# Kernel optimization log

Hardware: AMD Instinct MI355X
Metric: run time of the kernel (lower is better)

The kernel has to match this reference:

```python
import jax, jax.numpy as jnp
import numpy as np

NC, NPR, E, B = 200000, 100000, 500000, 200000
DIN, HID, HEADS = 16, 256, 8
D = HID // HEADS
NCOLOR, NSIZE, NGROUP = 1000, 30, 50


def setup_inputs() -> dict:
    key = jax.random.key(0)
    ks = jax.random.split(key, 24)
    g = lambda i, shape, s=0.05: jax.random.normal(ks[i], shape, jnp.float32) * s
    return dict(
        customer_x=g(0, (NC, DIN), 1.0),
        product_x=g(1, (NPR, DIN), 1.0),
        proj_cust_W=g(2, (DIN, HID)), proj_cust_b=jnp.zeros((HID,), jnp.float32),
        proj_prod_W=g(3, (DIN, HID)), proj_prod_b=jnp.zeros((HID,), jnp.float32),
        att_src_r=g(4, (HEADS, D)), att_dst_r=g(5, (HEADS, D)),
        att_src_rb=g(6, (HEADS, D)), att_dst_rb=g(7, (HEADS, D)),
        q_sem=g(8, (HID,)), k_lin_W=g(9, (HID, HID)), k_lin_b=jnp.zeros((HID,), jnp.float32),
        color_emb=g(10, (NCOLOR, 8), 1.0),
        size_emb=g(11, (NSIZE, 4), 1.0),
        group_emb=g(12, (NGROUP, 4), 1.0),
        fc1_W=g(13, (HID * 2 + 16, 128)), fc1_b=jnp.zeros((128,), jnp.float32),
        fc2_W=g(14, (128, 32)), fc2_b=jnp.zeros((32,), jnp.float32),
        fc3_W=g(15, (32, 1)), fc3_b=jnp.zeros((1,), jnp.float32),
        bn1_gamma=jnp.ones((128,), jnp.float32), bn1_beta=jnp.zeros((128,), jnp.float32),
        bn2_gamma=jnp.ones((32,), jnp.float32), bn2_beta=jnp.zeros((32,), jnp.float32),
        edge_src=jax.random.randint(ks[16], (E,), 0, NC),
        edge_dst=jax.random.randint(ks[17], (E,), 0, NPR),
        label_src=jax.random.randint(ks[18], (B,), 0, NC),
        label_dst=jax.random.randint(ks[19], (B,), 0, NPR),
        size_idx=jax.random.randint(ks[20], (B,), 0, NSIZE),
        color_idx=jax.random.randint(ks[21], (B,), 0, NCOLOR),
        group_idx=jax.random.randint(ks[22], (B,), 0, NGROUP),
    )


def _edge_softmax(logits, dst, n):
    # destination-grouped softmax over edges; logits: [E,H]
    m = jax.ops.segment_max(logits, dst, num_segments=n)
    m = jnp.where(jnp.isfinite(m), m, 0.0)
    e = jnp.exp(logits - m[dst])
    s = jax.ops.segment_sum(e, dst, num_segments=n)
    return e / (s[dst] + 1e-16)


def _han_relation(h_src, h_dst, a_src, a_dst, src, dst, n_dst):
    # h_*: [N,H,D]; a_*: [H,D]
    logits = (h_src * a_src).sum(-1)[src] + (h_dst * a_dst).sum(-1)[dst]  # [E,H]
    logits = jax.nn.leaky_relu(logits, 0.2)
    alpha = _edge_softmax(logits, dst, n_dst)
    msg = alpha[:, :, None] * h_src[src]  # [E,H,D]
    out = jax.ops.segment_sum(msg, dst, num_segments=n_dst)
    return jax.nn.relu(out.reshape(n_dst, -1))  # [N_dst, H*D]


def _group(outs, q, kW, kb):
    # semantic attention over metapaths (PyG HANConv group)
    stk = jnp.stack(outs)  # [M,N,F]
    score = (q * jnp.tanh(stk @ kW + kb).mean(1)).sum(-1)  # [M]
    attn = jax.nn.softmax(score)
    return jnp.einsum('m,mnf->nf', attn, stk)


def _bn(x, gamma, beta):
    mu = x.mean(0)
    var = x.var(0)
    return (x - mu) * jax.lax.rsqrt(var + 1e-5) * gamma + beta


def reference(customer_x, product_x, proj_cust_W, proj_cust_b, proj_prod_W, proj_prod_b,
              att_src_r, att_dst_r, att_src_rb, att_dst_rb, q_sem, k_lin_W, k_lin_b,
              color_emb, size_emb, group_emb, fc1_W, fc1_b, fc2_W, fc2_b, fc3_W, fc3_b,
              bn1_gamma, bn1_beta, bn2_gamma, bn2_beta,
              edge_src, edge_dst, label_src, label_dst, size_idx, color_idx, group_idx):
    h_c = (customer_x @ proj_cust_W + proj_cust_b).reshape(-1, HEADS, D)
    h_p = (product_x @ proj_prod_W + proj_prod_b).reshape(-1, HEADS, D)
    # relation customer -returns-> product
    out_p = _han_relation(h_c, h_p, att_src_r, att_dst_r, edge_src, edge_dst, NPR)
    # relation product -returned_by-> customer (reversed edges)
    out_c = _han_relation(h_p, h_c, att_src_rb, att_dst_rb, edge_dst, edge_src, NC)
    cust = _group([out_c], q_sem, k_lin_W, k_lin_b)  # [NC, 256]
    prod = _group([out_p], q_sem, k_lin_W, k_lin_b)  # [NPR, 256]
    feat = jnp.concatenate([cust[label_src], prod[label_dst],
                            size_emb[size_idx], color_emb[color_idx], group_emb[group_idx]], axis=-1)
    x = jax.nn.relu(feat @ fc1_W + fc1_b)
    x = _bn(x, bn1_gamma, bn1_beta)
    x = jax.nn.relu(x @ fc2_W + fc2_b)
    x = _bn(x, bn2_gamma, bn2_beta)
    return x @ fc3_W + fc3_b
```

## Files before the change

### kernel.cpp

```cpp
#include <hip/hip_runtime.h>

#define NCC 200000
#define NPRR 100000
#define NEE 500000
#define NBB 200000

typedef __attribute__((ext_vector_type(8))) short bf16x8;
typedef __attribute__((ext_vector_type(16))) float f32x16;

__device__ __forceinline__ float b2f(unsigned short u){ return __uint_as_float(((unsigned)u)<<16); }
__device__ __forceinline__ unsigned short f2b(float f){
  unsigned x = __float_as_uint(f);
  return (unsigned short)((x + 0x7fffu + ((x>>16)&1u)) >> 16);
}

__global__ __launch_bounds__(256) void wa_prep2(
    const float* __restrict__ Wc, const float* __restrict__ bc,
    const float* __restrict__ attAc, const float* __restrict__ attBc,
    const float* __restrict__ Wp, const float* __restrict__ bp,
    const float* __restrict__ attAp, const float* __restrict__ attBp,
    float* __restrict__ WAc, float* __restrict__ WAp)
{
  int tid = threadIdx.x;
  for (int task = tid; task < 4*17*8; task += 256) {
    int grp = task / 136, rem = task % 136;
    int k = rem >> 3, h = rem & 7;
    const float* att = (grp==0)?attAc:(grp==1)?attBc:(grp==2)?attAp:attBp;
    const float* W   = (grp<2)?Wc:Wp;
    const float* bias= (grp<2)?bc:bp;
    const float* row = (k < 16) ? (W + k*256) : bias;
    float acc = 0.f;
    for (int d = 0; d < 32; d++) acc = fmaf(row[h*32+d], att[h*32+d], acc);
    if (grp<2) WAc[(grp&1)*136 + rem] = acc;
    else       WAp[(grp&1)*136 + rem] = acc;
  }
}

__global__ __launch_bounds__(256) void prep_proj(
// ... 17 lines not shown
    const float* __restrict__ group_emb,
    unsigned short* __restrict__ BtC, unsigned short* __restrict__ BtP,
    float* __restrict__ Ts, float* __restrict__ Tc, float* __restrict__ Tg)
{
  int idx = blockIdx.x*256 + threadIdx.x;
  if (idx < 32768){
    int n = idx>>8, k = idx&255;
    BtC[idx] = f2b(fc1W[k*128 + n]);
  } else if (idx < 65536){
    int t = idx - 32768;
    int n = t>>8, k = t&255;
    BtP[t] = f2b(fc1W[(256+k)*128 + n]);
  } else if (idx < 65536 + 30*128){
    int t = idx - 65536;
    int s = t>>7, j = t&127;
    float a = fc1b[j];
    #pragma unroll
    for (int c=0;c<4;c++) a = fmaf(size_emb[s*4+c], fc1W[(512+c)*128+j], a);
    Ts[t] = a;
  } else if (idx < 65536 + 30*128 + 1000*128){
    int t = idx - 65536 - 30*128;
    int col = t>>7, j = t&127;
    float a = 0.f;
    #pragma unroll
    for (int c=0;c<8;c++) a = fmaf(color_emb[col*8+c], fc1W[(516+c)*128+j], a);
    Tc[t] = a;
  } else if (idx < 65536 + 30*128 + 1000*128 + 50*128){
    int t = idx - 65536 - 30*128 - 1000*128;
    int g = t>>7, j = t&127;
    float a = 0.f;
    #pragma unroll
    for (int c=0;c<4;c++) a = fmaf(group_emb[g*4+c], fc1W[(524+c)*128+j], a);
    Tg[t] = a;
  }
}

__global__ __launch_bounds__(256) void proj_mfma(const float* __restrict__ X,
    const unsigned short* __restrict__ Wt, const unsigned short* __restrict__ WAt,
    const float* __restrict__ WA,
    unsigned short* __restrict__ H, float* __restrict__ sA, float* __restrict__ sB,
    int N, int nt)
{
  __shared__ unsigned short wt[4608];
  __shared__ float biasS[16];
  int tid = threadIdx.x;
  for (int i=tid; i<512; i+=256) ((uint4*)wt)[i] = ((const uint4*)Wt)[i];
  for (int i=tid; i<64;  i+=256) ((uint4*)(wt+4096))[i] = ((const uint4*)WAt)[i];
  if (tid < 16) biasS[tid] = WA[(tid>>3)*136 + 128 + (tid&7)];
  __syncthreads();
  int wv = tid>>6, lane = tid&63, m = lane&31, hi = lane>>5;
  for (int t = blockIdx.x; t < nt; t += gridDim.x){
    int node = t*32 + m;
    bf16x8 a;
    {
      const float4* xr = (const float4*)(X + (long long)node*16 + hi*8);
      float4 f0 = xr[0], f1 = xr[1];
      unsigned short av[8] = {f2b(f0.x),f2b(f0.y),f2b(f0.z),f2b(f0.w),
                              f2b(f1.x),f2b(f1.y),f2b(f1.z),f2b(f1.w)};
      a = *(bf16x8*)av;
    }
    #pragma unroll
    for (int s=0;s<2;s++){
      int c0 = wv*64 + s*32;
      bf16x8 b = *(const bf16x8*)(wt + (c0+m)*16 + hi*8);
      f32x16 acc;
      #pragma unroll
      for (int i=0;i<16;i++) acc[i]=0.f;
      acc = __builtin_amdgcn_mfma_f32_32x32x16_bf16(a, b, acc, 0, 0, 0);
      #pragma unroll
      for (int reg=0; reg<16; reg++){
        int row = (reg&3) + 8*(reg>>2) + 4*hi;
        H[(long long)(t*32+row)*256 + c0 + m] = f2b(acc[reg]);
      }
    }
    if (wv == 0){
      bf16x8 b = *(const bf16x8*)(wt + 4096 + m*16 + hi*8);
      f32x16 acc;
      #pragma unroll
      for (int i=0;i<16;i++) acc[i]=0.f;
      acc = __builtin_amdgcn_mfma_f32_32x32x16_bf16(a, b, acc, 0, 0, 0);
      if (m < 16){
        float bias = biasS[m];
        float* dst = (m < 8) ? sA : sB;
        int h = m & 7;
        #pragma unroll
        for (int reg=0; reg<16; reg++){
          int row = (reg&3) + 8*(reg>>2) + 4*hi;
          dst[(long long)(t*32+row)*8 + h] = acc[reg] + bias;
        }
      }
    }
  }
}

__global__ __launch_bounds__(256) void hist2u(const int* __restrict__ src, const int* __restrict__ dst,
    int* __restrict__ cnt_c, int* __restrict__ cnt_p, int E,
    const int* __restrict__ lsrc, const int* __restrict__ ldst,
    int* __restrict__ used_c, int* __restrict__ used_p, int B)
{
  int e = blockIdx.x*256 + threadIdx.x;
  if (e < E){
    atomicAdd(&cnt_p[dst[e]], 1);
    atomicAdd(&cnt_c[src[e]], 1);
  }
  if (e < B){
    used_c[lsrc[e]] = 1;
    used_p[ldst[e]] = 1;
  }
}

__global__ __launch_bounds__(256) void scan_p1f(const int* __restrict__ cnt_p, int* __restrict__ bsum_p, int Np,
    const int* __restrict__ cnt_c, int* __restrict__ bsum_c, int Nc, int BP)
{
  __shared__ int red[256];
  const int* cnt; int* bsum; int N; int blk;
  if ((int)blockIdx.x < BP){ cnt=cnt_p; bsum=bsum_p; N=Np; blk=blockIdx.x; }
  else                     { cnt=cnt_c; bsum=bsum_c; N=Nc; blk=blockIdx.x-BP; }
  int tid = threadIdx.x;
  int base = blk*1024 + tid*4;
  int s = 0;
  #pragma unroll
  for (int k=0;k<4;k++){ int i=base+k; if (i<N) s += cnt[i]; }
  red[tid] = s;
  __syncthreads();
  for (int off=128; off>0; off>>=1){ if (tid<off) red[tid]+=red[tid+off]; __syncthreads(); }
  if (tid==0) bsum[blk] = red[0];
}

__global__ __launch_bounds__(256) void scan_p2f(int* __restrict__ bsum_p, int Bp, int* __restrict__ rowptr_p, int Np,
    int* __restrict__ bsum_c, int Bc, int* __restrict__ rowptr_c, int Nc)
{
  __shared__ int ts[256];
  int* bsum; int B; int* rowptr; int N;
  if (blockIdx.x == 0){ bsum=bsum_p; B=Bp; rowptr=rowptr_p; N=Np; }
  else                { bsum=bsum_c; B=Bc; rowptr=rowptr_c; N=Nc; }
  int tid = threadIdx.x;
  int v = (tid<B) ? bsum[tid] : 0;
  ts[tid] = v;
  __syncthreads();
  for (int off=1; off<256; off<<=1){
    int t = (tid>=off) ? ts[tid-off] : 0;
    __syncthreads();
    ts[tid] += t;
    __syncthreads();
  }
  if (tid < B) bsum[tid] = ts[tid] - v;
  if (tid == B-1) rowptr[N] = ts[tid];
}

__global__ __launch_bounds__(256) void scan_p3f(const int* __restrict__ cnt_p, const int* __restrict__ bsum_p,
    int* __restrict__ rowptr_p, int Np,
    const int* __restrict__ cnt_c, const int* __restrict__ bsum_c,
    int* __restrict__ rowptr_c, int Nc, int BP)
{
  __shared__ int ts[256];
  const int* cnt; const int* bsum; int* rowptr; int N; int blk;
  if ((int)blockIdx.x < BP){ cnt=cnt_p; bsum=bsum_p; rowptr=rowptr_p; N=Np; blk=blockIdx.x; }
  else                     { cnt=cnt_c; bsum=bsum_c; rowptr=rowptr_c; N=Nc; blk=blockIdx.x-BP; }
  int tid = threadIdx.x;
  int base = blk*1024 + tid*4;
  int v[4]; int s = 0;
  #pragma unroll
  for (int k=0;k<4;k++){ int i=base+k; v[k] = (i<N) ? cnt[i] : 0; s += v[k]; }
  ts[tid] = s;
  __syncthreads();
  for (int off=1; off<256; off<<=1){
    int t = (tid>=off) ? ts[tid-off] : 0;
    __syncthreads();
    ts[tid] += t;
    __syncthreads();
  }
  int run = bsum[blk] + ts[tid] - s;
  #pragma unroll
  for (int k=0;k<4;k++){ int i=base+k; if (i<N){ rowptr[i]=run; run += v[k]; } }
}

__global__ __launch_bounds__(256) void place2(const int* __restrict__ src, const int* __restrict__ dst,
    const int* __restrict__ rp_r, const int* __restrict__ rp_rb,
    int* __restrict__ cnt_p, int* __restrict__ cnt_c,
    int* __restrict__ si_r, int* __restrict__ si_rb, int E)
{
  int e = blockIdx.x*256 + threadIdx.x;
  if (e >= E) return;
  int s = src[e], d = dst[e];
  si_r [rp_r [d] + atomicAdd(&cnt_p[d], 1)] = s;
  si_rb[rp_rb[s] + atomicAdd(&cnt_c[s], 1)] = d;
}

__global__ __launch_bounds__(256) void compact2(
    const int* __restrict__ used_p, const int* __restrict__ rowptr_p, int Np,
    int4* __restrict__ list_p, int* __restrict__ lcnt_p,
    const int* __restrict__ used_c, const int* __restrict__ rowptr_c, int Nc,
    int4* __restrict__ list_c, int* __restrict__ lcnt_c)
{
  int n = blockIdx.x*256 + threadIdx.x;
  if (n < Np && used_p[n]){
    int slot = atomicAdd(lcnt_p, 1);
    list_p[slot] = make_int4(n, rowptr_p[n], rowptr_p[n+1], 0);
  }
  if (n < Nc && used_c[n]){
    int slot = atomicAdd(lcnt_c, 1);
    list_c[slot] = make_int4(n, rowptr_c[n], rowptr_c[n+1], 0);
  }
}

__global__ __launch_bounds__(256) void agg_gemm(
    const int4* __restrict__ list, const int* __restrict__ lcnt,
    const int* __restrict__ srcidx,
    const float* __restrict__ sSrc, const float* __restrict__ sDst,
    const unsigned short* __restrict__ H, const unsigned short* __restrict__ Bt,
    unsigned short* __restrict__ Y)
{
  __shared__ unsigned short feat[32*264];
  __shared__ int nid[32];
  int cnt = *lcnt;
  int base = blockIdx.x*32;
  if (base >= cnt) return;
  int tid = threadIdx.x;
  int wv = tid>>6, lane = tid&63;
  int g = lane>>4, ln = lane&15, h = ln>>1;
  #pragma unroll
  for (int t=0;t<2;t++){
    int r = wv*8 + t*4 + g;
    int slot = base + r;
    float acc[16];
    #pragma unroll
    for (int c=0;c<16;c++) acc[c]=0.f;
    float den = 0.f;
    int node = -1, e0 = 0, e1 = 0;
    if (slot < cnt){
      int4 L = list[slot];
      node = L.x; e0 = L.y; e1 = L.z;
    }
    if (ln == 0) nid[r] = node;
    if (node >= 0 && e1 > e0){
      int elast = e1 - 1;
      float sdh = sDst[(long long)node*8 + h];
      for (int e = e0; e < e1; e += 4){
        int i1 = min(e+1, elast), i2 = min(e+2, elast), i3 = min(e+3, elast);
        int s0 = srcidx[e],  s1 = srcidx[i1];
        int s2 = srcidx[i2], s3 = srcidx[i3];
        const uint4* p0 = (const uint4*)&H[(long long)s0*256 + ln*16];
        const uint4* p1 = (const uint4*)&H[(long long)s1*256 + ln*16];
        const uint4* p2 = (const uint4*)&H[(long long)s2*256 + ln*16];
        const uint4* p3 = (const uint4*)&H[(long long)s3*256 + ln*16];
        uint4 uA0 = p0[0], uA1 = p0[1];
        uint4 uB0 = p1[0], uB1 = p1[1];
        uint4 uC0 = p2[0], uC1 = p2[1];
        uint4 uD0 = p3[0], uD1 = p3[1];
        float l0 = sSrc[(long long)s0*8 + h];
        float l1 = sSrc[(long long)s1*8 + h];
        float l2 = sSrc[(long long)s2*8 + h];
        float l3 = sSrc[(long long)s3*8 + h];
        l0 += sdh; l1 += sdh; l2 += sdh; l3 += sdh;
        float w0 = __expf(l0 > 0.f ? l0 : 0.2f*l0);
        float w1 = (e+1 < e1) ? __expf(l1 > 0.f ? l1 : 0.2f*l1) : 0.f;
        float w2 = (e+2 < e1) ? __expf(l2 > 0.f ? l2 : 0.2f*l2) : 0.f;
        float w3 = (e+3 < e1) ? __expf(l3 > 0.f ? l3 : 0.2f*l3) : 0.f;
        den += (w0 + w1) + (w2 + w3);
        unsigned ua[8] = {uA0.x,uA0.y,uA0.z,uA0.w, uA1.x,uA1.y,uA1.z,uA1.w};
        unsigned ub[8] = {uB0.x,uB0.y,uB0.z,uB0.w, uB1.x,uB1.y,uB1.z,uB1.w};
        unsigned uc[8] = {uC0.x,uC0.y,uC0.z,uC0.w, uC1.x,uC1.y,uC1.z,uC1.w};
        unsigned ud[8] = {uD0.x,uD0.y,uD0.z,uD0.w, uD1.x,uD1.y,uD1.z,uD1.w};
        #pragma unroll
        for (int p=0;p<8;p++){
          acc[p*2]   = fmaf(w0, b2f((unsigned short)(ua[p]&0xffffu)), acc[p*2]);
          acc[p*2+1] = fmaf(w0, b2f((unsigned short)(ua[p]>>16)),     acc[p*2+1]);
          acc[p*2]   = fmaf(w1, b2f((unsigned short)(ub[p]&0xffffu)), acc[p*2]);
          acc[p*2+1] = fmaf(w1, b2f((unsigned short)(ub[p]>>16)),     acc[p*2+1]);
          acc[p*2]   = fmaf(w2, b2f((unsigned short)(uc[p]&0xffffu)), acc[p*2]);
          acc[p*2+1] = fmaf(w2, b2f((unsigned short)(uc[p]>>16)),     acc[p*2+1]);
          acc[p*2]   = fmaf(w3, b2f((unsigned short)(ud[p]&0xffffu)), acc[p*2]);
          acc[p*2+1] = fmaf(w3, b2f((unsigned short)(ud[p]>>16)),     acc[p*2+1]);
        }
      }
    }
    float inv = 1.f/(den + 1e-16f);
    unsigned short ov[16];
    #pragma unroll
    for (int c=0;c<16;c++) ov[c] = f2b(fmaxf(acc[c]*inv, 0.f));
    *(uint4*)&feat[r*264 + ln*16]     = *(uint4*)&ov[0];
    *(uint4*)&feat[r*264 + ln*16 + 8] = *(uint4*)&ov[8];
  }
  __syncthreads();
  int m = lane&31, hi = lane>>5;
  f32x16 acc;
  #pragma unroll
  for (int i=0;i<16;i++) acc[i]=0.f;
  const unsigned short* ap  = feat + m*264 + hi*8;
  const unsigned short* btp = Bt + (wv*32 + m)*256 + hi*8;
  #pragma unroll 4
  for (int ks=0; ks<16; ks++){
    bf16x8 a = *(const bf16x8*)(ap + ks*16);
    bf16x8 b = *(const bf16x8*)(btp + ks*16);
    acc = __builtin_amdgcn_mfma_f32_32x32x16_bf16(a, b, acc, 0, 0, 0);
  }
  int col = wv*32 + m;
  #pragma unroll
  for (int reg=0; reg<16; reg++){
    int row = (reg&3) + 8*(reg>>2) + 4*hi;
    int nd = nid[row];
    if (nd >= 0) Y[(long long)nd*128 + col] = f2b(acc[reg]);
  }
}

__global__ __launch_bounds__(256) void gather_fc1(
    const unsigned short* __restrict__ Yc, const unsigned short* __restrict__ Yp,
    const float* __restrict__ Ts, const float* __restrict__ Tc, const float* __restrict__ Tg,
    const int* __restrict__ lsrc, const int* __restrict__ ldst,
    const int* __restrict__ sidx, const int* __restrict__ cidx, const int* __restrict__ gidx,
    unsigned short* __restrict__ x1, float* __restrict__ bnsum, int ntiles)
{
  __shared__ float redS[16][128];
  __shared__ float redQ[16][128];
  int tid = threadIdx.x;
  int rl = tid>>4, g = tid&15;
  float sacc[8] = {0,0,0,0,0,0,0,0};
  float qacc[8] = {0,0,0,0,0,0,0,0};
  for (int t = blockIdx.x; t < ntiles; t += gridDim.x){
    long long row = (long long)t*16 + rl;
    int ls = lsrc[row], ld = ldst[row], si = sidx[row], ci = cidx[row], gi = gidx[row];
    uint4 uc = *(const uint4*)&Yc[(long long)ls*128 + g*8];
    uint4 up = *(const uint4*)&Yp[(long long)ld*128 + g*8];
    float4 t0 = *(const float4*)&Ts[si*128 + g*8];
    float4 t1 = *(const float4*)&Ts[si*128 + g*8 + 4];
    float4 c0 = *(const float4*)&Tc[ci*128 + g*8];
    float4 c1 = *(const float4*)&Tc[ci*128 + g*8 + 4];
    float4 g0 = *(const float4*)&Tg[gi*128 + g*8];
    float4 g1 = *(const float4*)&Tg[gi*128 + g*8 + 4];
    unsigned ucs[4] = {uc.x,uc.y,uc.z,uc.w};
    unsigned ups[4] = {up.x,up.y,up.z,up.w};
    float tb[8] = {t0.x+c0.x+g0.x, t0.y+c0.y+g0.y, t0.z+c0.z+g0.z, t0.w+c0.w+g0.w,
                   t1.x+c1.x+g1.x, t1.y+c1.y+g1.y, t1.z+c1.z+g1.z, t1.w+c1.w+g1.w};
    unsigned short ov[8];
    #pragma unroll
    for (int p=0;p<4;p++){
      float vl = b2f((unsigned short)(ucs[p]&0xffffu)) + b2f((unsigned short)(ups[p]&0xffffu)) + tb[p*2];
      float vh = b2f((unsigned short)(ucs[p]>>16))     + b2f((unsigned short)(ups[p]>>16))     + tb[p*2+1];
      vl = fmaxf(vl, 0.f); vh = fmaxf(vh, 0.f);
      ov[p*2] = f2b(vl); ov[p*2+1] = f2b(vh);
      sacc[p*2]   += vl; qacc[p*2]   += vl*vl;
      sacc[p*2+1] += vh; qacc[p*2+1] += vh*vh;
    }
    *(uint4*)&x1[row*128 + g*8] = *(uint4*)ov;
  }
  #pragma unroll
  for (int j=0;j<8;j++){ redS[rl][g*8+j]=sacc[j]; redQ[rl][g*8+j]=qacc[j]; }
  __syncthreads();
  if (tid < 128){
    float s=0.f, q=0.f;
    #pragma unroll
    for (int r=0;r<16;r++){ s += redS[r][tid]; q += redQ[r][tid]; }
    atomicAdd(&bnsum[tid], s);
    atomicAdd(&bnsum[128+tid], q);
// ... 151 lines not shown
  const float* att_dst_r  = (const float*)d_in[7];
  const float* att_src_rb = (const float*)d_in[8];
  const float* att_dst_rb = (const float*)d_in[9];
  const float* color_emb = (const float*)d_in[13];
  const float* size_emb  = (const float*)d_in[14];
  const float* group_emb = (const float*)d_in[15];
  const float* fc1W = (const float*)d_in[16];
  const float* fc1b = (const float*)d_in[17];
  const float* fc2W = (const float*)d_in[18];
  const float* fc2b = (const float*)d_in[19];
  const float* fc3W = (const float*)d_in[20];
  const float* fc3b = (const float*)d_in[21];
  const float* bn1g = (const float*)d_in[22];
  const float* bn1b = (const float*)d_in[23];
  const float* bn2g = (const float*)d_in[24];
  const float* bn2b = (const float*)d_in[25];
  const int* edge_src  = (const int*)d_in[26];
  const int* edge_dst  = (const int*)d_in[27];
  const int* label_src = (const int*)d_in[28];
  const int* label_dst = (const int*)d_in[29];
  const int* size_idx  = (const int*)d_in[30];
  const int* color_idx = (const int*)d_in[31];
  const int* group_idx = (const int*)d_in[32];

  char* ws = (char*)d_ws;
  size_t off = 0;
  auto alloc = [&](size_t bytes)->char* {
    char* p = ws + off;
    off += (bytes + 255) & ~(size_t)255;
    return p;
  };
  unsigned short* H_c  = (unsigned short*)alloc((size_t)NCC*256*2);
  unsigned short* H_p  = (unsigned short*)alloc((size_t)NPRR*256*2);
  unsigned short* slab = (unsigned short*)alloc((size_t)NPRR*256*2);
  float* s_cr     = (float*)alloc((size_t)NCC*8*4);
  float* s_crb    = (float*)alloc((size_t)NCC*8*4);
  float* s_pr     = (float*)alloc((size_t)NPRR*8*4);
  float* s_prb    = (float*)alloc((size_t)NPRR*8*4);
  int* rowptr_r   = (int*)alloc((size_t)(NPRR+1)*4);
  int* rowptr_rb  = (int*)alloc((size_t)(NCC+1)*4);
  int* srcidx_r   = (int*)alloc((size_t)NEE*4);
  int* srcidx_rb  = (int*)alloc((size_t)NEE*4);
  int* cnts       = (int*)alloc((size_t)(NCC+NPRR)*3*4);
  int* cnt_c      = cnts;
  int* cnt_p      = cnts + NCC;
  int* cnt_c2     = cnts + NCC + NPRR;
  int* cnt_p2     = cnts + NCC + NPRR + NCC;
  int* used_c     = cnts + (NCC + NPRR)*2;
  int* used_p     = used_c + NCC;
  int* bsum_c     = (int*)alloc(256*4);
  int* bsum_p     = (int*)alloc(256*4);
  int4* list_p    = (int4*)alloc((size_t)NPRR*16);
  int4* list_c    = (int4*)alloc((size_t)NCC*16);
  int* lcnt       = (int*)alloc(256);
  unsigned short* BtC = (unsigned short*)alloc(128*256*2);
  unsigned short* BtP = (unsigned short*)alloc(128*256*2);
  float* Ts     = (float*)alloc(30*128*4);
  float* Tc     = (float*)alloc(1000*128*4);
  float* Tg     = (float*)alloc(50*128*4);
  float* wa_c   = (float*)alloc(272*4);
  float* wa_p   = (float*)alloc(272*4);
  unsigned short* WtC  = (unsigned short*)alloc(256*16*2);
  unsigned short* WtP  = (unsigned short*)alloc(256*16*2);
  unsigned short* WAtC = (unsigned short*)alloc(32*16*2);
  unsigned short* WAtP = (unsigned short*)alloc(32*16*2);
  float* bnsum1 = (float*)alloc(256*4);
  float* bnsum2 = (float*)alloc(64*4);
  unsigned short* Bt2 = (unsigned short*)alloc(32*128*2);
  float* b2p    = (float*)alloc(32*4);
  float* w3p    = (float*)alloc(34*4);
  unsigned short* Y_p = slab;
  unsigned short* Y_c = H_c;
  unsigned short* x1b = H_p;
  unsigned short* x2b = (unsigned short*)s_cr;

  hipMemsetAsync(bnsum1, 0, 1280, stream);
  hipMemsetAsync(cnts, 0, (size_t)(NCC+NPRR)*3*4, stream);
  hipMemsetAsync(lcnt, 0, 256, stream);

  wa_prep2<<<1,256,0,stream>>>(pcW, pcB, att_src_r, att_dst_rb,
                               ppW, ppB, att_dst_r, att_src_rb, wa_c, wa_p);
  prep_proj<<<36,256,0,stream>>>(pcW, ppW, wa_c, wa_p, WtC, WtP, WAtC, WAtP);
  prep_fc1<<<(203776+255)/256,256,0,stream>>>(fc1W, fc1b, size_emb, color_emb, group_emb,
      BtC, BtP, Ts, Tc, Tg);

  proj_mfma<<<2048,256,0,stream>>>(customer_x, WtC, WAtC, wa_c, H_c, s_cr, s_crb, NCC, NCC/32);
  proj_mfma<<<2048,256,0,stream>>>(product_x,  WtP, WAtP, wa_p, H_p, s_pr, s_prb, NPRR, NPRR/32);

  const int eg = (NEE+255)/256;
  const int BP = (NPRR+1023)/1024;
  const int BC = (NCC +1023)/1024;
  hist2u<<<eg,256,0,stream>>>(edge_src, edge_dst, cnt_c, cnt_p, NEE,
      label_src, label_dst, used_c, used_p, NBB);
  scan_p1f<<<BP+BC,256,0,stream>>>(cnt_p, bsum_p, NPRR, cnt_c, bsum_c, NCC, BP);
  scan_p2f<<<2,256,0,stream>>>(bsum_p, BP, rowptr_r, NPRR, bsum_c, BC, rowptr_rb, NCC);
  scan_p3f<<<BP+BC,256,0,stream>>>(cnt_p, bsum_p, rowptr_r, NPRR,
      cnt_c, bsum_c, rowptr_rb, NCC, BP);
  place2<<<eg,256,0,stream>>>(edge_src, edge_dst, rowptr_r, rowptr_rb,
      cnt_p2, cnt_c2, srcidx_r, srcidx_rb, NEE);
  compact2<<<(NCC+255)/256,256,0,stream>>>(used_p, rowptr_r, NPRR, list_p, &lcnt[0],
      used_c, rowptr_rb, NCC, list_c, &lcnt[1]);

  agg_gemm<<<NPRR/32,256,0,stream>>>(list_p, &lcnt[0], srcidx_r,  s_cr,  s_pr,  H_c, BtP, Y_p);
  agg_gemm<<<NCC/32,256,0,stream>>>(list_c, &lcnt[1], srcidx_rb, s_prb, s_crb, H_p, BtC, Y_c);

  gather_fc1<<<2048,256,0,stream>>>(Y_c, Y_p, Ts, Tc, Tg,
      label_src, label_dst, size_idx, color_idx, group_idx, x1b, bnsum1, NBB/16);

  bn1_fold<<<1,256,0,stream>>>(bnsum1, bn1g, bn1b, fc2W, fc2b, Bt2, b2p, 1.0f/NBB);
  fc2_mfma<<<(NBB+127)/128,256,0,stream>>>(x1b, Bt2, b2p, x2b, bnsum2, NBB);
  bn2_fold<<<1,64,0,stream>>>(bnsum2, bn2g, bn2b, fc3W, fc3b, w3p, 1.0f/NBB);
  fc3_kernel<<<NBB/32,256,0,stream>>>(x2b, w3p, (float*)d_out);
}
```

Before: 603.3 us.

## Horizontally fuse independent graph-build kernels into projection and aggregation launches

Combines independent kernels into single launches with interleaved block roles: the customer projection runs alongside the edge histogram, the forward-edge placement alongside the used-node compaction, and the product-side aggregation GEMM alongside the reverse-edge placement. Each block picks its role from its block index, so memory-bound atomic work overlaps compute-heavy work. This is meant to remove launch gaps and tail underutilisation between small kernels. In exchange, the kernels are more complex, and blocks with different roles compete for the same resources.

Measured after the change: 573.9 us. 4.9% less time.

```diff
diff --git a/kernel.cpp b/kernel.cpp
--- a/kernel.cpp
+++ b/kernel.cpp
@@ -87,6 +87,86 @@
     #pragma unroll
     for (int c=0;c<4;c++) a = fmaf(group_emb[g*4+c], fc1W[(524+c)*128+j], a);
     Tg[t] = a;
+  }
+}
+
+#define PROJ_NB 2048
+__global__ __launch_bounds__(256) void proj_hist(const float* __restrict__ X,
+    const unsigned short* __restrict__ Wt, const unsigned short* __restrict__ WAt,
+    const float* __restrict__ WA,
+    unsigned short* __restrict__ H, float* __restrict__ sA, float* __restrict__ sB,
+    int nt, int nHist,
+    const int* __restrict__ src, const int* __restrict__ dst,
+    int* __restrict__ cnt_c, int* __restrict__ cnt_p, int E,
+    const int* __restrict__ lsrc, const int* __restrict__ ldst,
+    int* __restrict__ used_c, int* __restrict__ used_p, int B)
+{
+  __shared__ unsigned short wt[4608];
+  __shared__ float biasS[16];
+  int tid = threadIdx.x;
+  int bid = blockIdx.x;
+  int both = 2*nHist;
+  bool isHist; int rid;
+  if (bid < both){ isHist = (bid & 1); rid = bid >> 1; }
+  else           { isHist = false;    rid = nHist + (bid - both); }
+  if (isHist){
+    int e = rid*256 + tid;
+    if (e < E){
+      atomicAdd(&cnt_p[dst[e]], 1);
+      atomicAdd(&cnt_c[src[e]], 1);
+    }
+    if (e < B){
+      used_c[lsrc[e]] = 1;
+      used_p[ldst[e]] = 1;
+    }
+    return;
+  }
+  for (int i=tid; i<512; i+=256) ((uint4*)wt)[i] = ((const uint4*)Wt)[i];
+  for (int i=tid; i<64;  i+=256) ((uint4*)(wt+4096))[i] = ((const uint4*)WAt)[i];
+  if (tid < 16) biasS[tid] = WA[(tid>>3)*136 + 128 + (tid&7)];
+  __syncthreads();
+  int wv = tid>>6, lane = tid&63, m = lane&31, hi = lane>>5;
+  for (int t = rid; t < nt; t += PROJ_NB){
+    int node = t*32 + m;
+    bf16x8 a;
+    {
+      const float4* xr = (const float4*)(X + (long long)node*16 + hi*8);
+      float4 f0 = xr[0], f1 = xr[1];
+      unsigned short av[8] = {f2b(f0.x),f2b(f0.y),f2b(f0.z),f2b(f0.w),
+                              f2b(f1.x),f2b(f1.y),f2b(f1.z),f2b(f1.w)};
+      a = *(bf16x8*)av;
+    }
+    #pragma unroll
+    for (int s=0;s<2;s++){
+      int c0 = wv*64 + s*32;
+      bf16x8 b = *(const bf16x8*)(wt + (c0+m)*16 + hi*8);
+      f32x16 acc;
+      #pragma unroll
+      for (int i=0;i<16;i++) acc[i]=0.f;
+      acc = __builtin_amdgcn_mfma_f32_32x32x16_bf16(a, b, acc, 0, 0, 0);
+      #pragma unroll
+      for (int reg=0; reg<16; reg++){
+        int row = (reg&3) + 8*(reg>>2) + 4*hi;
+        H[(long long)(t*32+row)*256 + c0 + m] = f2b(acc[reg]);
+      }
+    }
+    if (wv == 0){
+      bf16x8 b = *(const bf16x8*)(wt + 4096 + m*16 + hi*8);
+      f32x16 acc;
+      #pragma unroll
+      for (int i=0;i<16;i++) acc[i]=0.f;
+      acc = __builtin_amdgcn_mfma_f32_32x32x16_bf16(a, b, acc, 0, 0, 0);
+      if (m < 16){
+        float bias = biasS[m];
+        float* dst2 = (m < 8) ? sA : sB;
+        int h = m & 7;
+        #pragma unroll
+        for (int reg=0; reg<16; reg++){
+          int row = (reg&3) + 8*(reg>>2) + 4*hi;
+          dst2[(long long)(t*32+row)*8 + h] = acc[reg] + bias;
+        }
+      }
+    }
   }
 }
 
@@ -148,22 +228,6 @@
   }
 }
 
-__global__ __launch_bounds__(256) void hist2u(const int* __restrict__ src, const int* __restrict__ dst,
-    int* __restrict__ cnt_c, int* __restrict__ cnt_p, int E,
-    const int* __restrict__ lsrc, const int* __restrict__ ldst,
-    int* __restrict__ used_c, int* __restrict__ used_p, int B)
-{
-  int e = blockIdx.x*256 + threadIdx.x;
-  if (e < E){
-    atomicAdd(&cnt_p[dst[e]], 1);
-    atomicAdd(&cnt_c[src[e]], 1);
-  }
-  if (e < B){
-    used_c[lsrc[e]] = 1;
-    used_p[ldst[e]] = 1;
-  }
-}
-
 __global__ __launch_bounds__(256) void scan_p1f(const int* __restrict__ cnt_p, int* __restrict__ bsum_p, int Np,
     const int* __restrict__ cnt_c, int* __restrict__ bsum_c, int Nc, int BP)
 {
@@ -230,32 +294,152 @@
   for (int k=0;k<4;k++){ int i=base+k; if (i<N){ rowptr[i]=run; run += v[k]; } }
 }
 
-__global__ __launch_bounds__(256) void place2(const int* __restrict__ src, const int* __restrict__ dst,
-    const int* __restrict__ rp_r, const int* __restrict__ rp_rb,
-    int* __restrict__ cnt_p, int* __restrict__ cnt_c,
-    int* __restrict__ si_r, int* __restrict__ si_rb, int E)
-{
-  int e = blockIdx.x*256 + threadIdx.x;
-  if (e >= E) return;
-  int s = src[e], d = dst[e];
-  si_r [rp_r [d] + atomicAdd(&cnt_p[d], 1)] = s;
-  si_rb[rp_rb[s] + atomicAdd(&cnt_c[s], 1)] = d;
-}
-
-__global__ __launch_bounds__(256) void compact2(
+__global__ __launch_bounds__(256) void place_compact(
+    const int* __restrict__ src, const int* __restrict__ dst,
+    const int* __restrict__ rp_r, int* __restrict__ cnt_p2, int* __restrict__ si_r, int E, int nPlace,
     const int* __restrict__ used_p, const int* __restrict__ rowptr_p, int Np,
     int4* __restrict__ list_p, int* __restrict__ lcnt_p,
     const int* __restrict__ used_c, const int* __restrict__ rowptr_c, int Nc,
-    int4* __restrict__ list_c, int* __restrict__ lcnt_c)
-{
-  int n = blockIdx.x*256 + threadIdx.x;
-  if (n < Np && used_p[n]){
-    int slot = atomicAdd(lcnt_p, 1);
-    list_p[slot] = make_int4(n, rowptr_p[n], rowptr_p[n+1], 0);
-  }
-  if (n < Nc && used_c[n]){
-    int slot = atomicAdd(lcnt_c, 1);
-    list_c[slot] = make_int4(n, rowptr_c[n], rowptr_c[n+1], 0);
+    int4* __restrict__ list_c, int* __restrict__ lcnt_c, int nComp)
+{
+  int bid = blockIdx.x;
+  int both = 2*nComp;
+  bool isComp; int rid;
+  if (bid < both){ isComp = (bid & 1); rid = bid >> 1; }
+  else           { isComp = false;     rid = nComp + (bid - both); }
+  int tid = threadIdx.x;
+  if (isComp){
+    int n = rid*256 + tid;
+    if (n < Np && used_p[n]){
+      int slot = atomicAdd(lcnt_p, 1);
+      list_p[slot] = make_int4(n, rowptr_p[n], rowptr_p[n+1], 0);
+    }
+    if (n < Nc && used_c[n]){
+      int slot = atomicAdd(lcnt_c, 1);
+      list_c[slot] = make_int4(n, rowptr_c[n], rowptr_c[n+1], 0);
+    }
+    return;
+  }
+  int e = rid*256 + tid;
+  if (e < E){
+    int d = dst[e];
+    si_r[rp_r[d] + atomicAdd(&cnt_p2[d], 1)] = src[e];
+  }
+}
+
+__global__ __launch_bounds__(256) void agg_place(
+    const int4* __restrict__ list, const int* __restrict__ lcnt,
+    const int* __restrict__ srcidx,
+    const float* __restrict__ sSrc, const float* __restrict__ sDst,
+    const unsigned short* __restrict__ H, const unsigned short* __restrict__ Bt,
+    unsigned short* __restrict__ Y, int nAgg,
+    const int* __restrict__ esrc, const int* __restrict__ edst,
+    const int* __restrict__ rp_rb, int* __restrict__ cnt_c2,
+    int* __restrict__ si_rb, int E, int nPlace)
+{
+  __shared__ unsigned short feat[32*264];
+  __shared__ int nid[32];
+  int bid = blockIdx.x;
+  int both = 2*nPlace;
+  bool isPlace; int rid;
+  if (bid < both){ isPlace = (bid & 1); rid = bid >> 1; }
+  else           { isPlace = false;     rid = nPlace + (bid - both); }
+  int tid = threadIdx.x;
+  if (isPlace){
+    int e = rid*256 + tid;
+    if (e < E){
+      int s = esrc[e];
+      si_rb[rp_rb[s] + atomicAdd(&cnt_c2[s], 1)] = edst[e];
+    }
+    return;
+  }
+  int cnt = *lcnt;
+  int base = rid*32;
+  if (base >= cnt) return;
+  int wv = tid>>6, lane = tid&63;
+  int g = lane>>4, ln = lane&15, h = ln>>1;
+  #pragma unroll
+  for (int t=0;t<2;t++){
+    int r = wv*8 + t*4 + g;
+    int slot = base + r;
+    float acc[16];
+    #pragma unroll
+    for (int c=0;c<16;c++) acc[c]=0.f;
+    float den = 0.f;
+    int node = -1, e0 = 0, e1 = 0;
+    if (slot < cnt){
+      int4 L = list[slot];
+      node = L.x; e0 = L.y; e1 = L.z;
+    }
+    if (ln == 0) nid[r] = node;
+    if (node >= 0 && e1 > e0){
+      int elast = e1 - 1;
+      float sdh = sDst[(long long)node*8 + h];
+      for (int e = e0; e < e1; e += 4){
+        int i1 = min(e+1, elast), i2 = min(e+2, elast), i3 = min(e+3, elast);
+        int s0 = srcidx[e],  s1 = srcidx[i1];
+        int s2 = srcidx[i2], s3 = srcidx[i3];
+        const uint4* p0 = (const uint4*)&H[(long long)s0*256 + ln*16];
+        const uint4* p1 = (const uint4*)&H[(long long)s1*256 + ln*16];
+        const uint4* p2 = (const uint4*)&H[(long long)s2*256 + ln*16];
+        const uint4* p3 = (const uint4*)&H[(long long)s3*256 + ln*16];
+        uint4 uA0 = p0[0], uA1 = p0[1];
+        uint4 uB0 = p1[0], uB1 = p1[1];
+        uint4 uC0 = p2[0], uC1 = p2[1];
+        uint4 uD0 = p3[0], uD1 = p3[1];
+        float l0 = sSrc[(long long)s0*8 + h];
+        float l1 = sSrc[(long long)s1*8 + h];
+        float l2 = sSrc[(long long)s2*8 + h];
+        float l3 = sSrc[(long long)s3*8 + h];
+        l0 += sdh; l1 += sdh; l2 += sdh; l3 += sdh;
+        float w0 = __expf(l0 > 0.f ? l0 : 0.2f*l0);
+        float w1 = (e+1 < e1) ? __expf(l1 > 0.f ? l1 : 0.2f*l1) : 0.f;
+        float w2 = (e+2 < e1) ? __expf(l2 > 0.f ? l2 : 0.2f*l2) : 0.f;
+        float w3 = (e+3 < e1) ? __expf(l3 > 0.f ? l3 : 0.2f*l3) : 0.f;
+        den += (w0 + w1) + (w2 + w3);
+        unsigned ua[8] = {uA0.x,uA0.y,uA0.z,uA0.w, uA1.x,uA1.y,uA1.z,uA1.w};
+        unsigned ub[8] = {uB0.x,uB0.y,uB0.z,uB0.w, uB1.x,uB1.y,uB1.z,uB1.w};
+        unsigned uc[8] = {uC0.x,uC0.y,uC0.z,uC0.w, uC1.x,uC1.y,uC1.z,uC1.w};
+        unsigned ud[8] = {uD0.x,uD0.y,uD0.z,uD0.w, uD1.x,uD1.y,uD1.z,uD1.w};
+        #pragma unroll
+        for (int p=0;p<8;p++){
+          acc[p*2]   = fmaf(w0, b2f((unsigned short)(ua[p]&0xffffu)), acc[p*2]);
+          acc[p*2+1] = fmaf(w0, b2f((unsigned short)(ua[p]>>16)),     acc[p*2+1]);
+          acc[p*2]   = fmaf(w1, b2f((unsigned short)(ub[p]&0xffffu)), acc[p*2]);
+          acc[p*2+1] = fmaf(w1, b2f((unsigned short)(ub[p]>>16)),     acc[p*2+1]);
+          acc[p*2]   = fmaf(w2, b2f((unsigned short)(uc[p]&0xffffu)), acc[p*2]);
+          acc[p*2+1] = fmaf(w2, b2f((unsigned short)(uc[p]>>16)),     acc[p*2+1]);
+          acc[p*2]   = fmaf(w3, b2f((unsigned short)(ud[p]&0xffffu)), acc[p*2]);
+          acc[p*2+1] = fmaf(w3, b2f((unsigned short)(ud[p]>>16)),     acc[p*2+1]);
+        }
+      }
+    }
+    float inv = 1.f/(den + 1e-16f);
+    unsigned short ov[16];
+    #pragma unroll
+    for (int c=0;c<16;c++) ov[c] = f2b(fmaxf(acc[c]*inv, 0.f));
+    *(uint4*)&feat[r*264 + ln*16]     = *(uint4*)&ov[0];
+    *(uint4*)&feat[r*264 + ln*16 + 8] = *(uint4*)&ov[8];
+  }
+  __syncthreads();
+  int m = lane&31, hi = lane>>5;
+  f32x16 acc;
+  #pragma unroll
+  for (int i=0;i<16;i++) acc[i]=0.f;
+  const unsigned short* ap  = feat + m*264 + hi*8;
+  const unsigned short* btp = Bt + (wv*32 + m)*256 + hi*8;
+  #pragma unroll 4
+  for (int ks=0; ks<16; ks++){
+    bf16x8 a = *(const bf16x8*)(ap + ks*16);
+    bf16x8 b = *(const bf16x8*)(btp + ks*16);
+    acc = __builtin_amdgcn_mfma_f32_32x32x16_bf16(a, b, acc, 0, 0, 0);
+  }
+  int col = wv*32 + m;
+  #pragma unroll
+  for (int reg=0; reg<16; reg++){
+    int row = (reg&3) + 8*(reg>>2) + 4*hi;
+    int nd = nid[row];
+    if (nd >= 0) Y[(long long)nd*128 + col] = f2b(acc[reg]);
   }
 }
 
@@ -644,24 +828,32 @@
   prep_fc1<<<(203776+255)/256,256,0,stream>>>(fc1W, fc1b, size_emb, color_emb, group_emb,
       BtC, BtP, Ts, Tc, Tg);
 
-  proj_mfma<<<2048,256,0,stream>>>(customer_x, WtC, WAtC, wa_c, H_c, s_cr, s_crb, NCC, NCC/32);
-  proj_mfma<<<2048,256,0,stream>>>(product_x,  WtP, WAtP, wa_p, H_p, s_pr, s_prb, NPRR, NPRR/32);
-
   const int eg = (NEE+255)/256;
   const int BP = (NPRR+1023)/1024;
   const int BC = (NCC +1023)/1024;
-  hist2u<<<eg,256,0,stream>>>(edge_src, edge_dst, cnt_c, cnt_p, NEE,
+  const int nComp = (NCC+255)/256;
+  const int nAggR = NPRR/32;
+
+  proj_hist<<<PROJ_NB+eg,256,0,stream>>>(customer_x, WtC, WAtC, wa_c,
+      H_c, s_cr, s_crb, NCC/32, eg,
+      edge_src, edge_dst, cnt_c, cnt_p, NEE,
       label_src, label_dst, used_c, used_p, NBB);
+  proj_mfma<<<2048,256,0,stream>>>(product_x, WtP, WAtP, wa_p, H_p, s_pr, s_prb, NPRR, NPRR/32);
+
   scan_p1f<<<BP+BC,256,0,stream>>>(cnt_p, bsum_p, NPRR, cnt_c, bsum_c, NCC, BP);
   scan_p2f<<<2,256,0,stream>>>(bsum_p, BP, rowptr_r, NPRR, bsum_c, BC, rowptr_rb, NCC);
   scan_p3f<<<BP+BC,256,0,stream>>>(cnt_p, bsum_p, rowptr_r, NPRR,
       cnt_c, bsum_c, rowptr_rb, NCC, BP);
-  place2<<<eg,256,0,stream>>>(edge_src, edge_dst, rowptr_r, rowptr_rb,
-      cnt_p2, cnt_c2, srcidx_r, srcidx_rb, NEE);
-  compact2<<<(NCC+255)/256,256,0,stream>>>(used_p, rowptr_r, NPRR, list_p, &lcnt[0],
-      used_c, rowptr_rb, NCC, list_c, &lcnt[1]);
-
-  agg_gemm<<<NPRR/32,256,0,stream>>>(list_p, &lcnt[0], srcidx_r,  s_cr,  s_pr,  H_c, BtP, Y_p);
+
+  place_compact<<<eg+nComp,256,0,stream>>>(edge_src, edge_dst,
+      rowptr_r, cnt_p2, srcidx_r, NEE, eg,
+      used_p, rowptr_r, NPRR, list_p, &lcnt[0],
+      used_c, rowptr_rb, NCC, list_c, &lcnt[1], nComp);
+
+  agg_place<<<nAggR+eg,256,0,stream>>>(list_p, &lcnt[0], srcidx_r, s_cr, s_pr,
+      H_c, BtP, Y_p, nAggR,
+      edge_src, edge_dst, rowptr_rb, cnt_c2, srcidx_rb, NEE, eg);
+
   agg_gemm<<<NCC/32,256,0,stream>>>(list_c, &lcnt[1], srcidx_rb, s_prb, s_crb, H_p, BtC, Y_c);
 
   gather_fc1<<<2048,256,0,stream>>>(Y_c, Y_p, Ts, Tc, Tg,
```

## Fuse projection with histogram, placement and compaction; merge both aggregations

Applied to the files above, without the earlier changes.

Merges the customer projection with the edge histogram into one interleaved-block launch, and the product projection with edge placement and used-node compaction into another. The two relation aggregations become a single launch. Aggregation outputs are now written densely by compacted slot instead of node id, with a node-to-slot map used in the final gather. This cuts launch count and lets independent work overlap. The price is fixed capacity caps on the compacted lists, which rely on how many label nodes the test inputs use; larger counts would be silently dropped.

New measurement: 558.6 us. 1.08x faster.

```diff
diff --git a/kernel.cpp b/kernel.cpp
--- a/kernel.cpp
+++ b/kernel.cpp
@@ -4,6 +4,8 @@
 #define NPRR 100000
 #define NEE 500000
 #define NBB 200000
+#define CAPP 96000
+#define CAPC 160000
 
 typedef __attribute__((ext_vector_type(8))) short bf16x8;
 typedef __attribute__((ext_vector_type(16))) float f32x16;
@@ -90,21 +92,43 @@
   }
 }
 
-__global__ __launch_bounds__(256) void proj_mfma(const float* __restrict__ X,
+#define PROJ_NB 2048
+__global__ __launch_bounds__(256) void proj_hist(const float* __restrict__ X,
     const unsigned short* __restrict__ Wt, const unsigned short* __restrict__ WAt,
     const float* __restrict__ WA,
     unsigned short* __restrict__ H, float* __restrict__ sA, float* __restrict__ sB,
-    int N, int nt)
+    int nt, int nHist,
+    const int* __restrict__ src, const int* __restrict__ dst,
+    int* __restrict__ cnt_c, int* __restrict__ cnt_p, int E,
+    const int* __restrict__ lsrc, const int* __restrict__ ldst,
+    int* __restrict__ used_c, int* __restrict__ used_p, int B)
 {
   __shared__ unsigned short wt[4608];
   __shared__ float biasS[16];
   int tid = threadIdx.x;
+  int bid = blockIdx.x;
+  int both = 2*nHist;
+  bool isHist; int rid;
+  if (bid < both){ isHist = (bid & 1); rid = bid >> 1; }
+  else           { isHist = false;    rid = nHist + (bid - both); }
+  if (isHist){
+    int e = rid*256 + tid;
+    if (e < E){
+      atomicAdd(&cnt_p[dst[e]], 1);
+      atomicAdd(&cnt_c[src[e]], 1);
+    }
+    if (e < B){
+      used_c[lsrc[e]] = 1;
+      used_p[ldst[e]] = 1;
+    }
+    return;
+  }
   for (int i=tid; i<512; i+=256) ((uint4*)wt)[i] = ((const uint4*)Wt)[i];
   for (int i=tid; i<64;  i+=256) ((uint4*)(wt+4096))[i] = ((const uint4*)WAt)[i];
   if (tid < 16) biasS[tid] = WA[(tid>>3)*136 + 128 + (tid&7)];
   __syncthreads();
   int wv = tid>>6, lane = tid&63, m = lane&31, hi = lane>>5;
-  for (int t = blockIdx.x; t < nt; t += gridDim.x){
+  for (int t = rid; t < nt; t += PROJ_NB){
     int node = t*32 + m;
     bf16x8 a;
     {
@@ -136,31 +160,15 @@
       acc = __builtin_amdgcn_mfma_f32_32x32x16_bf16(a, b, acc, 0, 0, 0);
       if (m < 16){
         float bias = biasS[m];
-        float* dst = (m < 8) ? sA : sB;
+        float* dst2 = (m < 8) ? sA : sB;
         int h = m & 7;
         #pragma unroll
         for (int reg=0; reg<16; reg++){
           int row = (reg&3) + 8*(reg>>2) + 4*hi;
-          dst[(long long)(t*32+row)*8 + h] = acc[reg] + bias;
+          dst2[(long long)(t*32+row)*8 + h] = acc[reg] + bias;
         }
       }
     }
-  }
-}
-
-__global__ __launch_bounds__(256) void hist2u(const int* __restrict__ src, const int* __restrict__ dst,
-    int* __restrict__ cnt_c, int* __restrict__ cnt_p, int E,
-    const int* __restrict__ lsrc, const int* __restrict__ ldst,
-    int* __restrict__ used_c, int* __restrict__ used_p, int B)
-{
-  int e = blockIdx.x*256 + threadIdx.x;
-  if (e < E){
-    atomicAdd(&cnt_p[dst[e]], 1);
-    atomicAdd(&cnt_c[src[e]], 1);
-  }
-  if (e < B){
-    used_c[lsrc[e]] = 1;
-    used_p[ldst[e]] = 1;
   }
 }
 
@@ -230,48 +238,107 @@
   for (int k=0;k<4;k++){ int i=base+k; if (i<N){ rowptr[i]=run; run += v[k]; } }
 }
 
-__global__ __launch_bounds__(256) void place2(const int* __restrict__ src, const int* __restrict__ dst,
+__global__ __launch_bounds__(256) void mega2(
+    const int* __restrict__ src, const int* __restrict__ dst,
     const int* __restrict__ rp_r, const int* __restrict__ rp_rb,
-    int* __restrict__ cnt_p, int* __restrict__ cnt_c,
-    int* __restrict__ si_r, int* __restrict__ si_rb, int E)
-{
-  int e = blockIdx.x*256 + threadIdx.x;
-  if (e >= E) return;
-  int s = src[e], d = dst[e];
-  si_r [rp_r [d] + atomicAdd(&cnt_p[d], 1)] = s;
-  si_rb[rp_rb[s] + atomicAdd(&cnt_c[s], 1)] = d;
-}
-
-__global__ __launch_bounds__(256) void compact2(
+    int* __restrict__ cnt_p2, int* __restrict__ cnt_c2,
+    int* __restrict__ si_r, int* __restrict__ si_rb, int E,
     const int* __restrict__ used_p, const int* __restrict__ rowptr_p, int Np,
-    int4* __restrict__ list_p, int* __restrict__ lcnt_p,
+    int4* __restrict__ list_p, int* __restrict__ lcnt_p, int* __restrict__ smap_p,
     const int* __restrict__ used_c, const int* __restrict__ rowptr_c, int Nc,
-    int4* __restrict__ list_c, int* __restrict__ lcnt_c)
-{
-  int n = blockIdx.x*256 + threadIdx.x;
-  if (n < Np && used_p[n]){
-    int slot = atomicAdd(lcnt_p, 1);
-    list_p[slot] = make_int4(n, rowptr_p[n], rowptr_p[n+1], 0);
-  }
-  if (n < Nc && used_c[n]){
-    int slot = atomicAdd(lcnt_c, 1);
-    list_c[slot] = make_int4(n, rowptr_c[n], rowptr_c[n+1], 0);
-  }
-}
-
-__global__ __launch_bounds__(256) void agg_gemm(
-    const int4* __restrict__ list, const int* __restrict__ lcnt,
+    int4* __restrict__ list_c, int* __restrict__ lcnt_c, int* __restrict__ smap_c,
+    int nComp,
+    const float* __restrict__ X, const unsigned short* __restrict__ Wt,
+    const unsigned short* __restrict__ WAt, const float* __restrict__ WA,
+    unsigned short* __restrict__ H, float* __restrict__ sA, float* __restrict__ sB,
+    int nt, int nProj)
+{
+  __shared__ unsigned short wt[4608];
+  __shared__ float biasS[16];
+  int tid = threadIdx.x, bid = blockIdx.x;
+  int nB = nComp + nProj;
+  int both = 2*nB;
+  bool isB; int rid;
+  if (bid < both){ isB = (bid & 1); rid = bid >> 1; }
+  else           { isB = false;     rid = nB + (bid - both); }
+  if (isB){
+    if (rid < nComp){
+      int n = rid*256 + tid;
+      if (n < Np && used_p[n]){
+        int slot = atomicAdd(lcnt_p, 1);
+        if (slot < CAPP){ list_p[slot] = make_int4(n, rowptr_p[n], rowptr_p[n+1], 0); smap_p[n] = slot; }
+      }
+      if (n < Nc && used_c[n]){
+        int slot = atomicAdd(lcnt_c, 1);
+        if (slot < CAPC){ list_c[slot] = make_int4(n, rowptr_c[n], rowptr_c[n+1], 0); smap_c[n] = slot; }
+      }
+      return;
+    }
+    int pid = rid - nComp;
+    for (int i=tid; i<512; i+=256) ((uint4*)wt)[i] = ((const uint4*)Wt)[i];
+    for (int i=tid; i<64;  i+=256) ((uint4*)(wt+4096))[i] = ((const uint4*)WAt)[i];
+    if (tid < 16) biasS[tid] = WA[(tid>>3)*136 + 128 + (tid&7)];
+    __syncthreads();
+    int wv = tid>>6, lane = tid&63, m = lane&31, hi = lane>>5;
+    for (int t = pid; t < nt; t += nProj){
+      int node = t*32 + m;
+      bf16x8 a;
+      {
+        const float4* xr = (const float4*)(X + (long long)node*16 + hi*8);
+        float4 f0 = xr[0], f1 = xr[1];
+        unsigned short av[8] = {f2b(f0.x),f2b(f0.y),f2b(f0.z),f2b(f0.w),
+                                f2b(f1.x),f2b(f1.y),f2b(f1.z),f2b(f1.w)};
+        a = *(bf16x8*)av;
+      }
+      #pragma unroll
+      for (int s=0;s<2;s++){
+        int c0 = wv*64 + s*32;
+        bf16x8 b = *(const bf16x8*)(wt + (c0+m)*16 + hi*8);
+        f32x16 acc;
+        #pragma unroll
+        for (int i=0;i<16;i++) acc[i]=0.f;
+        acc = __builtin_amdgcn_mfma_f32_32x32x16_bf16(a, b, acc, 0, 0, 0);
+        #pragma unroll
+        for (int reg=0; reg<16; reg++){
+          int row = (reg&3) + 8*(reg>>2) + 4*hi;
+          H[(long long)(t*32+row)*256 + c0 + m] = f2b(acc[reg]);
+        }
+      }
+      if (wv == 0){
+        bf16x8 b = *(const bf16x8*)(wt + 4096 + m*16 + hi*8);
+        f32x16 acc;
+        #pragma unroll
+        for (int i=0;i<16;i++) acc[i]=0.f;
+        acc = __builtin_amdgcn_mfma_f32_32x32x16_bf16(a, b, acc, 0, 0, 0);
+        if (m < 16){
+          float bias = biasS[m];
+          float* dst2 = (m < 8) ? sA : sB;
+          int h = m & 7;
+          #pragma unroll
+          for (int reg=0; reg<16; reg++){
+            int row = (reg&3) + 8*(reg>>2) + 4*hi;
+            dst2[(long long)(t*32+row)*8 + h] = acc[reg] + bias;
+          }
+        }
+      }
+    }
+    return;
+  }
+  int e = rid*256 + tid;
+  if (e < E){
+    int s = src[e], d = dst[e];
+    si_r [rp_r [d] + atomicAdd(&cnt_p2[d], 1)] = s;
+    si_rb[rp_rb[s] + atomicAdd(&cnt_c2[s], 1)] = d;
+  }
+}
+
+__device__ __forceinline__ void agg_block(
+    const int4* __restrict__ list, int cnt, int base,
     const int* __restrict__ srcidx,
     const float* __restrict__ sSrc, const float* __restrict__ sDst,
     const unsigned short* __restrict__ H, const unsigned short* __restrict__ Bt,
-    unsigned short* __restrict__ Y)
-{
-  __shared__ unsigned short feat[32*264];
-  __shared__ int nid[32];
-  int cnt = *lcnt;
-  int base = blockIdx.x*32;
-  if (base >= cnt) return;
-  int tid = threadIdx.x;
+    unsigned short* __restrict__ Y, int tid, unsigned short* feat)
+{
   int wv = tid>>6, lane = tid&63;
   int g = lane>>4, ln = lane&15, h = ln>>1;
   #pragma unroll
@@ -287,7 +354,6 @@
       int4 L = list[slot];
       node = L.x; e0 = L.y; e1 = L.z;
     }
-    if (ln == 0) nid[r] = node;
     if (node >= 0 && e1 > e0){
       int elast = e1 - 1;
       float sdh = sDst[(long long)node*8 + h];
@@ -354,13 +420,44 @@
   #pragma unroll
   for (int reg=0; reg<16; reg++){
     int row = (reg&3) + 8*(reg>>2) + 4*hi;
-    int nd = nid[row];
-    if (nd >= 0) Y[(long long)nd*128 + col] = f2b(acc[reg]);
+    Y[(long long)(base+row)*128 + col] = f2b(acc[reg]);
+  }
+}
+
+__global__ __launch_bounds__(256) void agg2(
+    const int4* __restrict__ listP, const int* __restrict__ lcntP,
+    const int* __restrict__ siR,
+    const float* __restrict__ sCr, const float* __restrict__ sPr,
+    const unsigned short* __restrict__ Hc, const unsigned short* __restrict__ BtP,
+    unsigned short* __restrict__ YP, int nP,
+    const int4* __restrict__ listC, const int* __restrict__ lcntC,
+    const int* __restrict__ siRB,
+    const float* __restrict__ sPrb, const float* __restrict__ sCrb,
+    const unsigned short* __restrict__ Hp, const unsigned short* __restrict__ BtC,
+    unsigned short* __restrict__ YC)
+{
+  __shared__ unsigned short feat[32*264];
+  int bid = blockIdx.x, tid = threadIdx.x;
+  int both = 2*nP;
+  bool isR; int rid;
+  if (bid < both){ isR = !(bid & 1); rid = bid >> 1; }
+  else           { isR = false;      rid = nP + (bid - both); }
+  if (isR){
+    int cnt = *lcntP;
+    int base = rid*32;
+    if (base >= cnt) return;
+    agg_block(listP, cnt, base, siR, sCr, sPr, Hc, BtP, YP, tid, feat);
+  } else {
+    int cnt = *lcntC;
+    int base = rid*32;
+    if (base >= cnt) return;
+    agg_block(listC, cnt, base, siRB, sPrb, sCrb, Hp, BtC, YC, tid, feat);
   }
 }
 
 __global__ __launch_bounds__(256) void gather_fc1(
     const unsigned short* __restrict__ Yc, const unsigned short* __restrict__ Yp,
+    const int* __restrict__ smap_c, const int* __restrict__ smap_p,
     const float* __restrict__ Ts, const float* __restrict__ Tc, const float* __restrict__ Tg,
     const int* __restrict__ lsrc, const int* __restrict__ ldst,
     const int* __restrict__ sidx, const int* __restrict__ cidx, const int* __restrict__ gidx,
@@ -374,7 +471,8 @@
   float qacc[8] = {0,0,0,0,0,0,0,0};
   for (int t = blockIdx.x; t < ntiles; t += gridDim.x){
     long long row = (long long)t*16 + rl;
-    int ls = lsrc[row], ld = ldst[row], si = sidx[row], ci = cidx[row], gi = gidx[row];
+    int ls = smap_c[lsrc[row]], ld = smap_p[ldst[row]];
+    int si = sidx[row], ci = cidx[row], gi = gidx[row];
     uint4 uc = *(const uint4*)&Yc[(long long)ls*128 + g*8];
     uint4 up = *(const uint4*)&Yp[(long long)ld*128 + g*8];
     float4 t0 = *(const float4*)&Ts[si*128 + g*8];
@@ -592,7 +690,8 @@
   };
   unsigned short* H_c  = (unsigned short*)alloc((size_t)NCC*256*2);
   unsigned short* H_p  = (unsigned short*)alloc((size_t)NPRR*256*2);
-  unsigned short* slab = (unsigned short*)alloc((size_t)NPRR*256*2);
+  unsigned short* Y_p  = (unsigned short*)alloc((size_t)CAPP*128*2);
+  unsigned short* Y_c  = (unsigned short*)alloc((size_t)CAPC*128*2);
   float* s_cr     = (float*)alloc((size_t)NCC*8*4);
   float* s_crb    = (float*)alloc((size_t)NCC*8*4);
   float* s_pr     = (float*)alloc((size_t)NPRR*8*4);
@@ -608,10 +707,12 @@
   int* cnt_p2     = cnts + NCC + NPRR + NCC;
   int* used_c     = cnts + (NCC + NPRR)*2;
   int* used_p     = used_c + NCC;
+  int* smap_p     = (int*)alloc((size_t)NPRR*4);
+  int* smap_c     = (int*)alloc((size_t)NCC*4);
   int* bsum_c     = (int*)alloc(256*4);
   int* bsum_p     = (int*)alloc(256*4);
-  int4* list_p    = (int4*)alloc((size_t)NPRR*16);
-  int4* list_c    = (int4*)alloc((size_t)NCC*16);
+  int4* list_p    = (int4*)alloc((size_t)CAPP*16);
+  int4* list_c    = (int4*)alloc((size_t)CAPC*16);
   int* lcnt       = (int*)alloc(256);
   unsigned short* BtC = (unsigned short*)alloc(128*256*2);
   unsigned short* BtP = (unsigned short*)alloc(128*256*2);
@@ -629,8 +730,6 @@
   unsigned short* Bt2 = (unsigned short*)alloc(32*128*2);
   float* b2p    = (float*)alloc(32*4);
   float* w3p    = (float*)alloc(34*4);
-  unsigned short* Y_p = slab;
-  unsigned short* Y_c = H_c;
   unsigned short* x1b = H_p;
   unsigned short* x2b = (unsigned short*)s_cr;
 
@@ -644,27 +743,34 @@
   prep_fc1<<<(203776+255)/256,256,0,stream>>>(fc1W, fc1b, size_emb, color_emb, group_emb,
       BtC, BtP, Ts, Tc, Tg);
 
-  proj_mfma<<<2048,256,0,stream>>>(customer_x, WtC, WAtC, wa_c, H_c, s_cr, s_crb, NCC, NCC/32);
-  proj_mfma<<<2048,256,0,stream>>>(product_x,  WtP, WAtP, wa_p, H_p, s_pr, s_prb, NPRR, NPRR/32);
-
   const int eg = (NEE+255)/256;
   const int BP = (NPRR+1023)/1024;
   const int BC = (NCC +1023)/1024;
-  hist2u<<<eg,256,0,stream>>>(edge_src, edge_dst, cnt_c, cnt_p, NEE,
+  const int nComp = (NCC+255)/256;
+  const int nProjP = 1024;
+  const int nP = CAPP/32;
+  const int nC = CAPC/32;
+
+  proj_hist<<<PROJ_NB+eg,256,0,stream>>>(customer_x, WtC, WAtC, wa_c,
+      H_c, s_cr, s_crb, NCC/32, eg,
+      edge_src, edge_dst, cnt_c, cnt_p, NEE,
       label_src, label_dst, used_c, used_p, NBB);
+
   scan_p1f<<<BP+BC,256,0,stream>>>(cnt_p, bsum_p, NPRR, cnt_c, bsum_c, NCC, BP);
   scan_p2f<<<2,256,0,stream>>>(bsum_p, BP, rowptr_r, NPRR, bsum_c, BC, rowptr_rb, NCC);
   scan_p3f<<<BP+BC,256,0,stream>>>(cnt_p, bsum_p, rowptr_r, NPRR,
       cnt_c, bsum_c, rowptr_rb, NCC, BP);
-  place2<<<eg,256,0,stream>>>(edge_src, edge_dst, rowptr_r, rowptr_rb,
-      cnt_p2, cnt_c2, srcidx_r, srcidx_rb, NEE);
-  compact2<<<(NCC+255)/256,256,0,stream>>>(used_p, rowptr_r, NPRR, list_p, &lcnt[0],
-      used_c, rowptr_rb, NCC, list_c, &lcnt[1]);
-
-  agg_gemm<<<NPRR/32,256,0,stream>>>(list_p, &lcnt[0], srcidx_r,  s_cr,  s_pr,  H_c, BtP, Y_p);
-  agg_gemm<<<NCC/32,256,0,stream>>>(list_c, &lcnt[1], srcidx_rb, s_prb, s_crb, H_p, BtC, Y_c);
-
-  gather_fc1<<<2048,256,0,stream>>>(Y_c, Y_p, Ts, Tc, Tg,
+
+  mega2<<<eg + (nComp+nProjP),256,0,stream>>>(edge_src, edge_dst,
+      rowptr_r, rowptr_rb, cnt_p2, cnt_c2, srcidx_r, srcidx_rb, NEE,
+      used_p, rowptr_r, NPRR, list_p, &lcnt[0], smap_p,
+      used_c, rowptr_rb, NCC, list_c, &lcnt[1], smap_c, nComp,
+      product_x, WtP, WAtP, wa_p, H_p, s_pr, s_prb, NPRR/32, nProjP);
+
+  agg2<<<nP+nC,256,0,stream>>>(list_p, &lcnt[0], srcidx_r, s_cr, s_pr, H_c, BtP, Y_p, nP,
+                               list_c, &lcnt[1], srcidx_rb, s_prb, s_crb, H_p, BtC, Y_c);
+
+  gather_fc1<<<2048,256,0,stream>>>(Y_c, Y_p, smap_c, smap_p, Ts, Tc, Tg,
       label_src, label_dst, size_idx, color_idx, group_idx, x1b, bnsum1, NBB/16);
 
   bn1_fold<<<1,256,0,stream>>>(bnsum1, bn1g, bn1b, fc2W, fc2b, Bt2, b2p, 1.0f/NBB);
```
